# Performance work log

Measured on AMD Instinct MI355X. Metric: run time of the kernel, lower is better.

The kernel has to match this reference:

```python
import jax, jax.numpy as jnp
import numpy as np

STRIDE = 2
PAD = 1
K = 4
OUT_PAD = 0


def setup_inputs() -> dict:
    key = jax.random.key(0)
    k1, k2, k3, k4 = jax.random.split(key, 4)
    x = jax.random.normal(k1, (16, 64, 128, 128), dtype=jnp.float32)
    # torch ConvTranspose2d weight layout: [in_channels, out_channels, kH, kW]
    w = jax.random.normal(k2, (64, 32, 4, 4), dtype=jnp.float32) * 0.05
    conv_b = jax.random.normal(k3, (32,), dtype=jnp.float32) * 0.05
    bias = jax.random.normal(k4, (1, 1, 1, 1), dtype=jnp.float32)
    return {"x": x, "w": w, "conv_b": conv_b, "bias": bias}


def conv_transpose2d(x, w, conv_b):
    # Equivalent of torch ConvTranspose2d(k=4, s=2, p=1, op=0):
    # dilate input by stride, pad by k-1-p (+op on trailing side), conv with flipped kernel.
    lo = K - 1 - PAD
    hi = K - 1 - PAD + OUT_PAD
    w_oihw = jnp.flip(w, axis=(2, 3)).transpose(1, 0, 2, 3)  # [Cout, Cin, kH, kW]
    y = jax.lax.conv_general_dilated(
        x, w_oihw,
        window_strides=(1, 1),
        padding=((lo, hi), (lo, hi)),
        lhs_dilation=(STRIDE, STRIDE),
        dimension_numbers=("NCHW", "OIHW", "NCHW"),
    )
    return y + conv_b[None, :, None, None]


def reference(x, w, conv_b, bias):
    y = conv_transpose2d(x, w, conv_b)          # [N, Cout, H', W']
    y = jnp.min(y, axis=1, keepdims=True)       # channel-min -> [N,1,H',W']
    y = jnp.sum(y, axis=2, keepdims=True)       # height-sum  -> [N,1,1,W']
    # kernel uses tanh-based GELU approximation
    return jax.nn.gelu(y, approximate=True) + bias
```

## Files before the change

### kernel.cpp

```cpp
#include <hip/hip_runtime.h>
#include <math.h>

typedef __attribute__((ext_vector_type(8))) short short8;
typedef __attribute__((ext_vector_type(16))) float f32x16;
typedef __attribute__((ext_vector_type(4))) unsigned uintx4;

#define XS_STRIDE 72
#define NROWS 6

__device__ __forceinline__ short f2bf(float f) {
    union { float f; unsigned u; } v; v.f = f;
    unsigned r = (v.u + 0x7FFFu + ((v.u >> 16) & 1u)) >> 16;
    return (short)r;
}

__device__ __forceinline__ unsigned cvt_pk_bf16(float lo, float hi) {
    unsigned r;
    asm("v_cvt_pk_bf16_f32 %0, %1, %2" : "=v"(r) : "v"(lo), "v"(hi));
    return r;
}

__device__ __forceinline__ void bar_lds() {
    asm volatile("s_waitcnt lgkmcnt(0)" ::: "memory");
    __builtin_amdgcn_s_barrier();
}

__global__ void prep(const float* __restrict__ w, short* __restrict__ wfrag,
                     float* __restrict__ acc, unsigned* __restrict__ ctr) {
    if (blockIdx.x >= 128) {
        #pragma unroll
        for (int i = 0; i < 16; ++i) acc[i * 256 + threadIdx.x] = 0.f;
        if (threadIdx.x < 16) ctr[threadIdx.x] = 0u;
        return;
    }
    int idx = blockIdx.x * 256 + threadIdx.x;
    int j    = idx & 7;
    int lane = (idx >> 3) & 63;
    int q    = (idx >> 9) & 15;
    int p    = idx >> 13;
    int co = lane & 31, hf = lane >> 5;
    int ci = (q & 3) * 16 + hf * 8 + j;
    int tq = q >> 2, a = tq >> 1, b = tq & 1;
    int ph = p >> 1, pw = p & 1;
    int kh = 2 * a + 1 - ph, kw = 2 * b + 1 - pw;
    wfrag[idx] = f2bf(w[((ci * 32 + co) * 4 + kh) * 4 + kw]);
}

__global__ __launch_bounds__(256, 2) void convt_mfma(
    const float* __restrict__ x, const short* __restrict__ wfrag,
    const float* __restrict__ conv_b, float* __restrict__ acc,
    unsigned* __restrict__ ctr, const float* __restrict__ bias,
    float* __restrict__ out)
{
    __shared__ short xs[NROWS][66][XS_STRIDE];
    __shared__ float minbuf[4][64];
    __shared__ unsigned lastf;

    int blk = ((blockIdx.x & 7) << 7) | (blockIdx.x >> 3);
    const int jh = blk & 1, st = (blk >> 1) & 31, n = blk >> 6;
    const int t  = threadIdx.x;
    const int i0 = st * 4;

    const int wv = t >> 6, lane = t & 63;
    const int ph = wv >> 1, pw = wv & 1;
    const int ln = lane & 31, half = lane >> 5;

    const float* xn = x + (size_t)n * 64 * 128 * 128;
    const int col  = t & 63;
    const int cib  = (t >> 6) * 16;
    const int gcol = jh * 64 + col;

    float pfA[16], pfB[16];
    auto load_row = [&](int r, float* dst) {
        int gi = i0 - 1 + r;
        bool rowok = (unsigned)gi < 128u;
        int gic = rowok ? gi : 0;
        const float* px = xn + ((size_t)cib * 128 + gic) * 128 + gcol;
        #pragma unroll
        for (int c = 0; c < 16; ++c) dst[c] = rowok ? px[c * 16384] : 0.f;
    };
    auto write_row = [&](int r, const float* src) {
        uintx4 u0, u1;
        u0.x = cvt_pk_bf16(src[0], src[1]);   u0.y = cvt_pk_bf16(src[2], src[3]);
        u0.z = cvt_pk_bf16(src[4], src[5]);   u0.w = cvt_pk_bf16(src[6], src[7]);
        u1.x = cvt_pk_bf16(src[8], src[9]);   u1.y = cvt_pk_bf16(src[10], src[11]);
        u1.z = cvt_pk_bf16(src[12], src[13]); u1.w = cvt_pk_bf16(src[14], src[15]);
        *(uintx4*)&xs[r][col + 1][cib]     = u0;
        *(uintx4*)&xs[r][col + 1][cib + 8] = u1;
    };
    load_row(0, pfA);
    load_row(1, pfB);
    write_row(0, pfA); load_row(2, pfA);
    write_row(1, pfB); load_row(3, pfB);
    write_row(2, pfA); load_row(4, pfA);
    write_row(3, pfB); load_row(5, pfB);
    write_row(4, pfA);
    write_row(5, pfB);

    float hv[3];
    #pragma unroll
    for (int q = 0; q < 3; ++q) {
        int idx = q * 256 + t;
        int r = idx >> 7, side = (idx >> 6) & 1, ci = idx & 63;
        int gi = i0 - 1 + r;
        int gc = jh * 64 + (side ? 64 : -1);
        hv[q] = ((unsigned)gi < 128u && (unsigned)gc < 128u)
              ? xn[((size_t)ci * 128 + gi) * 128 + gc] : 0.f;
    }
    #pragma unroll
    for (int q = 0; q < 3; ++q) {
        int idx = q * 256 + t;
        int r = idx >> 7, side = (idx >> 6) & 1, ci = idx & 63;
        xs[r][side ? 65 : 0][ci] = f2bf(hv[q]);
    }

    short8 af[16];
    {
        const short8* wf = (const short8*)(wfrag + wv * 8192);
        #pragma unroll
        for (int q = 0; q < 16; ++q) af[q] = wf[q * 64 + lane];
    }
    float cb[16];
    #pragma unroll
    for (int reg = 0; reg < 16; ++reg)
        cb[reg] = conv_b[(reg & 3) + 8 * (reg >> 2) + 4 * half];

    bar_lds();

    float osum0 = 0.f, osum1 = 0.f;
    #pragma unroll
    for (int k = 0; k < 2; ++k) {
        const int L0 = 2 * k + ph;
        #pragma unroll
        for (int jb = 0; jb < 2; ++jb) {
            f32x16 acc0, acc1;
            #pragma unroll
            for (int reg = 0; reg < 16; ++reg) { acc0[reg] = cb[reg]; acc1[reg] = cb[reg]; }
            __builtin_amdgcn_s_setprio(1);
            #pragma unroll
            for (int b = 0; b < 2; ++b) {
                int colp = jb * 32 + ln + (pw - b) + 1;
                const short* p0 = &xs[L0][colp][half * 8];
                const short* p1 = &xs[L0 + 1][colp][half * 8];
                const short* p2 = &xs[L0 + 2][colp][half * 8];
                #pragma unroll
                for (int c = 0; c < 4; ++c) {
                    short8 Fs = *(const short8*)(p1 + c * 16);
                    acc0 = __builtin_amdgcn_mfma_f32_32x32x16_bf16(af[4*b+c],   Fs, acc0, 0, 0, 0);
                    acc1 = __builtin_amdgcn_mfma_f32_32x32x16_bf16(af[8+4*b+c], Fs, acc1, 0, 0, 0);
                    short8 F0 = *(const short8*)(p0 + c * 16);
                    acc0 = __builtin_amdgcn_mfma_f32_32x32x16_bf16(af[8+4*b+c], F0, acc0, 0, 0, 0);
                    short8 F2 = *(const short8*)(p2 + c * 16);
                    acc1 = __builtin_amdgcn_mfma_f32_32x32x16_bf16(af[4*b+c],   F2, acc1, 0, 0, 0);
                }
            }
            __builtin_amdgcn_s_setprio(0);

            float mn0, mn1;
            {
                float a = fminf(fminf(acc0[0], acc0[1]), fminf(acc0[2], acc0[3]));
                float b2 = fminf(fminf(acc0[4], acc0[5]), fminf(acc0[6], acc0[7]));
                float c = fminf(fminf(acc0[8], acc0[9]), fminf(acc0[10], acc0[11]));
                float d = fminf(fminf(acc0[12], acc0[13]), fminf(acc0[14], acc0[15]));
                mn0 = fminf(fminf(a, b2), fminf(c, d));
                a = fminf(fminf(acc1[0], acc1[1]), fminf(acc1[2], acc1[3]));
                b2 = fminf(fminf(acc1[4], acc1[5]), fminf(acc1[6], acc1[7]));
                c = fminf(fminf(acc1[8], acc1[9]), fminf(acc1[10], acc1[11]));
                d = fminf(fminf(acc1[12], acc1[13]), fminf(acc1[14], acc1[15]));
                mn1 = fminf(fminf(a, b2), fminf(c, d));
            }
            mn0 = fminf(mn0, __shfl_xor(mn0, 32, 64));
            mn1 = fminf(mn1, __shfl_xor(mn1, 32, 64));
            if (jb == 0) osum0 += mn0 + mn1;
            else         osum1 += mn0 + mn1;
        }
    }

    if (half == 0) { minbuf[wv][ln] = osum0; minbuf[wv][32 + ln] = osum1; }
    bar_lds();

    if (t < 128) {
        int c = t & 63, pwp = (t >> 6) & 1;
        float v = minbuf[pwp][c] + minbuf[2 + pwp][c];
        int ow = ((jh * 64 + c) << 1) | pwp;
        atomicAdd(&acc[n * 256 + ow], v);
    }
    __syncthreads();
    if (t == 0) lastf = (atomicAdd(&ctr[n], 1u) == 63u) ? 1u : 0u;
    __syncthreads();

    if (lastf) {
        __threadfence();
        float s = __hip_atomic_load(&acc[n * 256 + t], __ATOMIC_RELAXED,
                                    __HIP_MEMORY_SCOPE_AGENT);
        float u = 0.7978845608028654f * (s + 0.044715f * s * s * s);
        out[n * 256 + t] = 0.5f * s * (1.f + tanhf(u)) + bias[0];
    }
}

extern "C" void kernel_launch(void* const* d_in, const int* in_sizes, int n_in,
                              void* d_out, int out_size, void* d_ws, size_t ws_size,
                              hipStream_t stream) {
    const float* x      = (const float*)d_in[0];
    const float* w      = (const float*)d_in[1];
    const float* conv_b = (const float*)d_in[2];
    const float* bias   = (const float*)d_in[3];
    float* out = (float*)d_out;

    short*    wfrag = (short*)d_ws;
    float*    acc   = (float*)((char*)d_ws + 65536);
    unsigned* ctr   = (unsigned*)((char*)d_ws + 65536 + 16384);

    hipLaunchKernelGGL(prep, dim3(129), dim3(256), 0, stream, w, wfrag, acc, ctr);
    hipLaunchKernelGGL(convt_mfma, dim3(16 * 32 * 2), dim3(256), 0, stream,
                       x, wfrag, conv_b, acc, ctr, bias, out);
}
```

Measured before the change: 115.1 us.

## Widen conv-transpose tile to full 128-column rows, removing halo loads

Each block now covers all 128 input columns of a 4-row strip instead of half, so the grid halves to 512 blocks. The left and right halo columns become the zero padding, which removes the global halo loads. Overlap re-reads of neighbouring column tiles also go away. In exchange, shared memory grows to about 112 KB of dynamic LDS and each thread holds 32-float prefetch buffers, which likely limits occupancy to one block per CU and leaves fewer blocks to hide latency.

```diff
diff --git a/kernel.cpp b/kernel.cpp
--- a/kernel.cpp
+++ b/kernel.cpp
@@ -5,7 +5,7 @@
 typedef __attribute__((ext_vector_type(16))) float f32x16;
 typedef __attribute__((ext_vector_type(4))) unsigned uintx4;
 
-#define XS_STRIDE 72
+#define XSTR 72
 #define NROWS 6
 
 __device__ __forceinline__ short f2bf(float f) {
@@ -52,12 +52,12 @@
     unsigned* __restrict__ ctr, const float* __restrict__ bias,
     float* __restrict__ out)
 {
-    __shared__ short xs[NROWS][66][XS_STRIDE];
-    __shared__ float minbuf[4][64];
+    extern __shared__ short xs[];
+    __shared__ float minbuf[4][128];
     __shared__ unsigned lastf;
 
-    int blk = ((blockIdx.x & 7) << 7) | (blockIdx.x >> 3);
-    const int jh = blk & 1, st = (blk >> 1) & 31, n = blk >> 6;
+    int blk = ((blockIdx.x & 7) << 6) | (blockIdx.x >> 3);
+    const int n = blk >> 5, st = blk & 31;
     const int t  = threadIdx.x;
     const int i0 = st * 4;
 
@@ -66,27 +66,29 @@
     const int ln = lane & 31, half = lane >> 5;
 
     const float* xn = x + (size_t)n * 64 * 128 * 128;
-    const int col  = t & 63;
-    const int cib  = (t >> 6) * 16;
-    const int gcol = jh * 64 + col;
-
-    float pfA[16], pfB[16];
+    const int col = t & 127;
+    const int cib = (t >> 7) * 32;
+
+    float pfA[32], pfB[32];
     auto load_row = [&](int r, float* dst) {
         int gi = i0 - 1 + r;
-        bool rowok = (unsigned)gi < 128u;
-        int gic = rowok ? gi : 0;
-        const float* px = xn + ((size_t)cib * 128 + gic) * 128 + gcol;
-        #pragma unroll
-        for (int c = 0; c < 16; ++c) dst[c] = rowok ? px[c * 16384] : 0.f;
+        bool ok = (unsigned)gi < 128u;
+        int gic = ok ? gi : 0;
+        const float* px = xn + (size_t)cib * 16384 + gic * 128 + col;
+        #pragma unroll
+        for (int c = 0; c < 32; ++c) dst[c] = ok ? px[c * 16384] : 0.f;
     };
     auto write_row = [&](int r, const float* src) {
-        uintx4 u0, u1;
-        u0.x = cvt_pk_bf16(src[0], src[1]);   u0.y = cvt_pk_bf16(src[2], src[3]);
-        u0.z = cvt_pk_bf16(src[4], src[5]);   u0.w = cvt_pk_bf16(src[6], src[7]);
-        u1.x = cvt_pk_bf16(src[8], src[9]);   u1.y = cvt_pk_bf16(src[10], src[11]);
-        u1.z = cvt_pk_bf16(src[12], src[13]); u1.w = cvt_pk_bf16(src[14], src[15]);
-        *(uintx4*)&xs[r][col + 1][cib]     = u0;
-        *(uintx4*)&xs[r][col + 1][cib + 8] = u1;
+        short* dp = &xs[((size_t)r * 130 + col + 1) * XSTR + cib];
+        #pragma unroll
+        for (int g = 0; g < 4; ++g) {
+            uintx4 u;
+            u.x = cvt_pk_bf16(src[g*8+0], src[g*8+1]);
+            u.y = cvt_pk_bf16(src[g*8+2], src[g*8+3]);
+            u.z = cvt_pk_bf16(src[g*8+4], src[g*8+5]);
+            u.w = cvt_pk_bf16(src[g*8+6], src[g*8+7]);
+            *(uintx4*)(dp + g * 8) = u;
+        }
     };
     load_row(0, pfA);
     load_row(1, pfB);
@@ -97,21 +99,11 @@
     write_row(4, pfA);
     write_row(5, pfB);
 
-    float hv[3];
-    #pragma unroll
-    for (int q = 0; q < 3; ++q) {
-        int idx = q * 256 + t;
-        int r = idx >> 7, side = (idx >> 6) & 1, ci = idx & 63;
-        int gi = i0 - 1 + r;
-        int gc = jh * 64 + (side ? 64 : -1);
-        hv[q] = ((unsigned)gi < 128u && (unsigned)gc < 128u)
-              ? xn[((size_t)ci * 128 + gi) * 128 + gc] : 0.f;
-    }
-    #pragma unroll
-    for (int q = 0; q < 3; ++q) {
-        int idx = q * 256 + t;
-        int r = idx >> 7, side = (idx >> 6) & 1, ci = idx & 63;
-        xs[r][side ? 65 : 0][ci] = f2bf(hv[q]);
+    if (t < 32) {
+        int side = t >> 4, c4 = (t & 15) * 4;
+        #pragma unroll
+        for (int r = 0; r < NROWS; ++r)
+            *(unsigned long long*)&xs[((size_t)r * 130 + (side ? 129 : 0)) * XSTR + c4] = 0ULL;
     }
 
     short8 af[16];
@@ -127,12 +119,12 @@
 
     bar_lds();
 
-    float osum0 = 0.f, osum1 = 0.f;
+    float osum[4] = {0.f, 0.f, 0.f, 0.f};
     #pragma unroll
     for (int k = 0; k < 2; ++k) {
         const int L0 = 2 * k + ph;
         #pragma unroll
-        for (int jb = 0; jb < 2; ++jb) {
+        for (int jb = 0; jb < 4; ++jb) {
             f32x16 acc0, acc1;
             #pragma unroll
             for (int reg = 0; reg < 16; ++reg) { acc0[reg] = cb[reg]; acc1[reg] = cb[reg]; }
@@ -140,9 +132,9 @@
             #pragma unroll
             for (int b = 0; b < 2; ++b) {
                 int colp = jb * 32 + ln + (pw - b) + 1;
-                const short* p0 = &xs[L0][colp][half * 8];
-                const short* p1 = &xs[L0 + 1][colp][half * 8];
-                const short* p2 = &xs[L0 + 2][colp][half * 8];
+                const short* p0 = &xs[((size_t)(L0    ) * 130 + colp) * XSTR + half * 8];
+                const short* p1 = &xs[((size_t)(L0 + 1) * 130 + colp) * XSTR + half * 8];
+                const short* p2 = &xs[((size_t)(L0 + 2) * 130 + colp) * XSTR + half * 8];
                 #pragma unroll
                 for (int c = 0; c < 4; ++c) {
                     short8 Fs = *(const short8*)(p1 + c * 16);
@@ -171,22 +163,24 @@
             }
             mn0 = fminf(mn0, __shfl_xor(mn0, 32, 64));
             mn1 = fminf(mn1, __shfl_xor(mn1, 32, 64));
-            if (jb == 0) osum0 += mn0 + mn1;
-            else         osum1 += mn0 + mn1;
+            osum[jb] += mn0 + mn1;
         }
     }
 
-    if (half == 0) { minbuf[wv][ln] = osum0; minbuf[wv][32 + ln] = osum1; }
+    if (half == 0) {
+        #pragma unroll
+        for (int jb = 0; jb < 4; ++jb) minbuf[wv][jb * 32 + ln] = osum[jb];
+    }
     bar_lds();
 
-    if (t < 128) {
-        int c = t & 63, pwp = (t >> 6) & 1;
+    {
+        int c = t & 127, pwp = t >> 7;
         float v = minbuf[pwp][c] + minbuf[2 + pwp][c];
-        int ow = ((jh * 64 + c) << 1) | pwp;
+        int ow = (c << 1) | pwp;
         atomicAdd(&acc[n * 256 + ow], v);
     }
     __syncthreads();
-    if (t == 0) lastf = (atomicAdd(&ctr[n], 1u) == 63u) ? 1u : 0u;
+    if (t == 0) lastf = (atomicAdd(&ctr[n], 1u) == 31u) ? 1u : 0u;
     __syncthreads();
 
     if (lastf) {
@@ -212,6 +206,7 @@
     unsigned* ctr   = (unsigned*)((char*)d_ws + 65536 + 16384);
 
     hipLaunchKernelGGL(prep, dim3(129), dim3(256), 0, stream, w, wfrag, acc, ctr);
-    hipLaunchKernelGGL(convt_mfma, dim3(16 * 32 * 2), dim3(256), 0, stream,
+    hipLaunchKernelGGL(convt_mfma, dim3(512), dim3(256),
+                       NROWS * 130 * XSTR * sizeof(short), stream,
                        x, wfrag, conv_b, acc, ctr, bias, out);
 }
```

After: 154.0 us. 33.8% more time.
